# Optimization experiments

Measured on AMD Instinct MI355X. Metric: run time of the kernel, lower is better.

Reference implementation:

```python
import jax, jax.numpy as jnp
import numpy as np

D_IN, D_HID = 64, 128

def _ff(x, w1, b1, w2, b2):
    # FeedForward: Linear -> ReLU -> Linear
    return jax.nn.relu(x @ w1 + b1) @ w2 + b2

def setup_inputs() -> dict:
    key = jax.random.key(0)
    ks = jax.random.split(key, 10)
    N, m = 8, 2048
    def lin(k, fan_in, fan_out):
        bound = 1.0 / np.sqrt(fan_in)
        return jax.random.uniform(k, (fan_in, fan_out), jnp.float32, -bound, bound)
    return {
        "x": jax.random.normal(ks[0], (N, m, D_IN), jnp.float32),
        "edge": jax.random.uniform(ks[1], (N, m, m), jnp.float32),
        # f: dim_in -> dim_hid//2 -> dim_hid
        "f_w1": lin(ks[2], D_IN, D_HID // 2),
        "f_b1": jnp.zeros((D_HID // 2,), jnp.float32),
        "f_w2": lin(ks[3], D_HID // 2, D_HID),
        "f_b2": jnp.zeros((D_HID,), jnp.float32),
        # g: 2*dim_in -> dim_hid -> dim_hid
        "g_w1": lin(ks[4], 2 * D_IN, D_HID),
        "g_b1": jnp.zeros((D_HID,), jnp.float32),
        "g_w2": lin(ks[5], D_HID, D_HID),
        "g_b2": jnp.zeros((D_HID,), jnp.float32),
    }

def reference(x, edge, f_w1, f_b1, f_w2, f_b2, g_w1, g_b1, g_w2, g_b2):
    # self dynamics: f(x) -> [N, m, D_HID]
    self_dyn = _ff(x, f_w1, f_b1, f_w2, f_b2)
    # Original builds interaction[n,i,j] = cat(x[n,i], x[n,i]) (receiver is
    # transposed twice), so g is constant along j. Compute g once per sender node.
    gx = _ff(jnp.concatenate([x, x], axis=-1), g_w1, g_b1, g_w2, g_b2)  # [N, m, H]
    # interaction.sum over sender dim i with edge weights: out[n,j] = sum_i edge[n,i,j]*gx[n,i]
    inter = jnp.einsum('nij,nih->njh', edge, gx)
    return self_dyn + inter
```

## Files before the change

kernel.cpp:

```cpp
#include <hip/hip_runtime.h>


typedef __attribute__((ext_vector_type(8))) short bf16x8;
typedef __attribute__((ext_vector_type(4))) unsigned short u16x4;
typedef __attribute__((ext_vector_type(4))) float f32x4;

static __device__ __forceinline__ unsigned short f2bf(float f) {
  union { float f; unsigned int i; } c; c.f = f;
  return (unsigned short)((c.i + 0x7fffu + ((c.i >> 16) & 1u)) >> 16);
}

__global__ __launch_bounds__(256) void k_gx(
    const float* __restrict__ x,
    const float* __restrict__ gw1,
    const float* __restrict__ gb1,
    const float* __restrict__ gw2,
    const float* __restrict__ gb2,
    unsigned short* __restrict__ gxT)
{
  __shared__ short xs[64 * 64];
  __shared__ short w1T[128 * 64];
  __shared__ short w2T[128 * 128];
  __shared__ short h2s[64 * 128];

  const int t = threadIdx.x;
  const int R0 = blockIdx.x * 64;

  for (int idx = t; idx < 64 * 128; idx += 256) {
    int k = idx >> 7, n = idx & 127;
    float v = gw1[idx] + gw1[64 * 128 + idx];
    w1T[(n << 6) + (((k >> 3) ^ (n & 7)) << 3) + (k & 7)] = (short)f2bf(v);
  }
  for (int idx = t; idx < 128 * 128; idx += 256) {
    int k = idx >> 7, n = idx & 127;
    w2T[(n << 7) + (((k >> 3) ^ (n & 7)) << 3) + (k & 7)] = (short)f2bf(gw2[idx]);
  }
  for (int s = t; s < 64 * 16; s += 256) {
    int row = s >> 4, c4 = s & 15;
    f32x4 v = *(const f32x4*)(x + (size_t)(R0 + row) * 64 + c4 * 4);
    u16x4 pk;
#pragma unroll
    for (int r = 0; r < 4; ++r) pk[r] = f2bf(v[r]);
    *(u16x4*)(xs + (row << 6) + (((c4 >> 1) ^ (row & 7)) << 3) + ((c4 & 1) << 2)) = pk;
  }
  __syncthreads();

  const int w = t >> 6, l = t & 63;
  const int lr = l & 15, q = l >> 4;
  const int mrow = w * 16 + lr;

  bf16x8 a[2];
#pragma unroll
  for (int ks = 0; ks < 2; ++ks) {
    int c = ks * 4 + q;
    a[ks] = *(const bf16x8*)(xs + (mrow << 6) + ((c ^ (mrow & 7)) << 3));
  }

  f32x4 acc;
#pragma unroll
  for (int nf = 0; nf < 8; ++nf) {
    acc = (f32x4){0.f, 0.f, 0.f, 0.f};
#pragma unroll
    for (int ks = 0; ks < 2; ++ks) {
      int c = ks * 4 + q;
      int nr = nf * 16 + lr;
      bf16x8 b = *(const bf16x8*)(w1T + (nr << 6) + ((c ^ (nr & 7)) << 3));
      acc = __builtin_amdgcn_mfma_f32_16x16x32_bf16(a[ks], b, acc, 0, 0, 0);
    }
    float bias = gb1[nf * 16 + lr];
#pragma unroll
    for (int r = 0; r < 4; ++r) {
      float v = acc[r] + bias;
      v = v > 0.f ? v : 0.f;
      int row = w * 16 + q * 4 + r, n = nf * 16 + lr;
      h2s[(row << 7) + (((n >> 3) ^ (row & 7)) << 3) + (n & 7)] = (short)f2bf(v);
    }
  }
  __syncthreads();

  bf16x8 a2[4];
#pragma unroll
  for (int ks = 0; ks < 4; ++ks) {
    int c = ks * 4 + q;
    a2[ks] = *(const bf16x8*)(h2s + (mrow << 7) + ((c ^ (mrow & 7)) << 3));
  }
  const int batch = R0 >> 11;
  const int ib = R0 & 2047;
#pragma unroll
  for (int nf = 0; nf < 8; ++nf) {
    acc = (f32x4){0.f, 0.f, 0.f, 0.f};
#pragma unroll
    for (int ks = 0; ks < 4; ++ks) {
      int c = ks * 4 + q;
      int nr = nf * 16 + lr;
      bf16x8 b = *(const bf16x8*)(w2T + (nr << 7) + ((c ^ (nr & 7)) << 3));
      acc = __builtin_amdgcn_mfma_f32_16x16x32_bf16(a2[ks], b, acc, 0, 0, 0);
    }
    float bias = gb2[nf * 16 + lr];
    u16x4 pk;
#pragma unroll
    for (int r = 0; r < 4; ++r) pk[r] = f2bf(acc[r] + bias);
    *(u16x4*)(gxT + (size_t)(batch * 128 + nf * 16 + lr) * 2048 + ib + w * 16 + q * 4) = pk;
  }
}

__global__ __launch_bounds__(256, 4) void k_main(
    const float* __restrict__ edge,
    const unsigned short* __restrict__ gxT,
    const float* __restrict__ x,
    const float* __restrict__ fw1,
    const float* __restrict__ fb1,
    const float* __restrict__ fw2,
    const float* __restrict__ fb2,
    float* __restrict__ out)
{
  __shared__ short eT[2][16 * 72];
  __shared__ short bT[128 * 64];
  __shared__ short xs[16 * 64];
  __shared__ short w1T[64 * 64];
  __shared__ short h1s[16 * 64];

  const int t = threadIdx.x;
  const int batch = blockIdx.x & 7;
  const int j0 = (blockIdx.x >> 3) * 16;

  const int w = t >> 6, l = t & 63;
  const int lr = l & 15, q = l >> 4;

  const int e_ii = t >> 2;
  const int e_cj = t & 3;

  const float* ep = edge + (size_t)batch * 2048 * 2048 + (size_t)e_ii * 2048 + j0 + e_cj * 4;
  const unsigned short* gp = gxT + ((size_t)batch * 128 + w * 32 + lr) * 2048 + q * 8;

  f32x4 acc[2];
#pragma unroll
  for (int nf = 0; nf < 2; ++nf) acc[nf] = (f32x4){0.f, 0.f, 0.f, 0.f};

  auto lde = [&](int kk, f32x4& er) {
    er = *(const f32x4*)(ep + (size_t)kk * 64 * 2048);
  };
  auto ldg = [&](int kk, bf16x8 gf[4]) {
    const unsigned short* p = gp + kk * 64;
#pragma unroll
    for (int nf = 0; nf < 2; ++nf)
#pragma unroll
      for (int ks = 0; ks < 2; ++ks)
        gf[nf * 2 + ks] = *(const bf16x8*)(p + nf * 16 * 2048 + ks * 32);
  };
  auto st_e = [&](int buf, const f32x4& er) {
#pragma unroll
    for (int u = 0; u < 4; ++u) {
      int jj = e_cj * 4 + u;
      eT[buf][jj * 72 + (((e_ii >> 3) ^ (jj >> 3)) << 3) + (e_ii & 7)] = (short)f2bf(er[u]);
    }
  };
  auto comp = [&](int buf, const bf16x8 gf[4]) {
#pragma unroll
    for (int ks = 0; ks < 2; ++ks) {
      const int c = ks * 4 + q;
      bf16x8 a = *(const bf16x8*)(&eT[buf][lr * 72 + ((c ^ (lr >> 3)) << 3)]);
#pragma unroll
      for (int nf = 0; nf < 2; ++nf)
        acc[nf] = __builtin_amdgcn_mfma_f32_16x16x32_bf16(a, gf[nf * 2 + ks], acc[nf], 0, 0, 0);
    }
  };

  f32x4 erA, erB;
  bf16x8 gfA[4], gfB[4];

  lde(0, erA);
  ldg(0, gfA);
  lde(1, erB);
  st_e(0, erA);
  __syncthreads();

#pragma unroll 1
  for (int mm = 0; mm < 15; ++mm) {
    ldg(2 * mm + 1, gfB);
    lde(2 * mm + 2, erA);
    comp(0, gfA);
    st_e(1, erB);
    __syncthreads();
    ldg(2 * mm + 2, gfA);
    lde(2 * mm + 3, erB);
    comp(1, gfB);
    st_e(0, erA);
    __syncthreads();
  }
  ldg(31, gfB);
  comp(0, gfA);
  st_e(1, erB);
  __syncthreads();
  comp(1, gfB);

  for (int idx = t; idx < 64 * 64; idx += 256) {
    int k = idx >> 6, n = idx & 63;
    w1T[(n << 6) + (((k >> 3) ^ (n & 7)) << 3) + (k & 7)] = (short)f2bf(fw1[idx]);
  }
  for (int idx = t; idx < 64 * 128; idx += 256) {
    int k = idx >> 7, n = idx & 127;
    bT[(n << 6) + (((k >> 3) ^ (n & 7)) << 3) + (k & 7)] = (short)f2bf(fw2[idx]);
  }
  {
    int s = t;
    int row = s >> 4, c4 = s & 15;
    f32x4 v = *(const f32x4*)(x + (size_t)(batch * 2048 + j0 + row) * 64 + c4 * 4);
    u16x4 pk;
#pragma unroll
    for (int r = 0; r < 4; ++r) pk[r] = f2bf(v[r]);
    *(u16x4*)(xs + (row << 6) + (((c4 >> 1) ^ (row & 7)) << 3) + ((c4 & 1) << 2)) = pk;
  }
  __syncthreads();

  if (w == 0) {
    bf16x8 a1[2];
#pragma unroll
    for (int ks = 0; ks < 2; ++ks) {
      int c = ks * 4 + q;
      a1[ks] = *(const bf16x8*)(xs + (lr << 6) + ((c ^ (lr & 7)) << 3));
    }
#pragma unroll
    for (int nf = 0; nf < 4; ++nf) {
      f32x4 h = (f32x4){0.f, 0.f, 0.f, 0.f};
#pragma unroll
      for (int ks = 0; ks < 2; ++ks) {
        int c = ks * 4 + q;
        int nr = nf * 16 + lr;
        bf16x8 b = *(const bf16x8*)(w1T + (nr << 6) + ((c ^ (nr & 7)) << 3));
        h = __builtin_amdgcn_mfma_f32_16x16x32_bf16(a1[ks], b, h, 0, 0, 0);
      }
      float bias = fb1[nf * 16 + lr];
#pragma unroll
      for (int r = 0; r < 4; ++r) {
        float v = h[r] + bias;
        v = v > 0.f ? v : 0.f;
        int row = q * 4 + r, n = nf * 16 + lr;
        h1s[(row << 6) + (((n >> 3) ^ (row & 7)) << 3) + (n & 7)] = (short)f2bf(v);
      }
    }
  }
  __syncthreads();

  bf16x8 a2[2];
#pragma unroll
  for (int ks = 0; ks < 2; ++ks) {
    int c = ks * 4 + q;
    a2[ks] = *(const bf16x8*)(h1s + (lr << 6) + ((c ^ (lr & 7)) << 3));
  }
#pragma unroll
  for (int nf = 0; nf < 2; ++nf) {
    int h = w * 32 + nf * 16 + lr;
#pragma unroll
    for (int ks = 0; ks < 2; ++ks) {
      int c = ks * 4 + q;
      bf16x8 b = *(const bf16x8*)(bT + (h << 6) + ((c ^ (h & 7)) << 3));
      acc[nf] = __builtin_amdgcn_mfma_f32_16x16x32_bf16(a2[ks], b, acc[nf], 0, 0, 0);
    }
    float bias = fb2[h];
#pragma unroll
    for (int r = 0; r < 4; ++r) {
      size_t o = ((size_t)batch * 2048 + j0 + q * 4 + r) * 128 + h;
      out[o] = acc[nf][r] + bias;
    }
  }
}

extern "C" void kernel_launch(void* const* d_in, const int* in_sizes, int n_in,
                              void* d_out, int out_size, void* d_ws, size_t ws_size,
                              hipStream_t stream) {
  const float* x    = (const float*)d_in[0];
  const float* edge = (const float*)d_in[1];
  const float* fw1  = (const float*)d_in[2];
  const float* fb1  = (const float*)d_in[3];
  const float* fw2  = (const float*)d_in[4];
  const float* fb2  = (const float*)d_in[5];
  const float* gw1  = (const float*)d_in[6];
  const float* gb1  = (const float*)d_in[7];
  const float* gw2  = (const float*)d_in[8];
  const float* gb2  = (const float*)d_in[9];
  float* out = (float*)d_out;

  unsigned short* gxT = (unsigned short*)d_ws;

  hipLaunchKernelGGL(k_gx, dim3(256), dim3(256), 0, stream, x, gw1, gb1, gw2, gb2, gxT);
  hipLaunchKernelGGL(k_main, dim3(1024), dim3(256), 0, stream, edge, gxT, x,
                     fw1, fb1, fw2, fb2, out);
}
```

Before: 281.4 us.

## Store gx in MFMA fragment order, vectorize weight loads, lighten barriers, raise MFMA priority

The k_gx kernel now writes gx in a pre-swizzled fragment layout, so each lane in k_main reads its bf16x8 operands with fully contiguous, coalesced loads instead of strided rows. Weight staging in k_gx uses float4 loads. The pipeline barriers in k_main drop __syncthreads for an LDS-only waitcnt plus s_barrier, so outstanding global loads are not drained at each barrier, and MFMA sections run at raised wave priority. The risk is that the lighter barrier depends on the producer and consumer layouts staying exactly consistent.

```diff
diff --git a/kernel.cpp b/kernel.cpp
--- a/kernel.cpp
+++ b/kernel.cpp
@@ -9,6 +9,11 @@
   union { float f; unsigned int i; } c; c.f = f;
   return (unsigned short)((c.i + 0x7fffu + ((c.i >> 16) & 1u)) >> 16);
 }
+
+#define LBAR() do { \
+  asm volatile("s_waitcnt lgkmcnt(0)" ::: "memory"); \
+  __builtin_amdgcn_s_barrier(); \
+} while (0)
 
 __global__ __launch_bounds__(256) void k_gx(
     const float* __restrict__ x,
@@ -16,7 +21,7 @@
     const float* __restrict__ gb1,
     const float* __restrict__ gw2,
     const float* __restrict__ gb2,
-    unsigned short* __restrict__ gxT)
+    unsigned short* __restrict__ gxF)
 {
   __shared__ short xs[64 * 64];
   __shared__ short w1T[128 * 64];
@@ -26,14 +31,24 @@
   const int t = threadIdx.x;
   const int R0 = blockIdx.x * 64;
 
-  for (int idx = t; idx < 64 * 128; idx += 256) {
-    int k = idx >> 7, n = idx & 127;
-    float v = gw1[idx] + gw1[64 * 128 + idx];
-    w1T[(n << 6) + (((k >> 3) ^ (n & 7)) << 3) + (k & 7)] = (short)f2bf(v);
-  }
-  for (int idx = t; idx < 128 * 128; idx += 256) {
-    int k = idx >> 7, n = idx & 127;
-    w2T[(n << 7) + (((k >> 3) ^ (n & 7)) << 3) + (k & 7)] = (short)f2bf(gw2[idx]);
+  for (int idx4 = t; idx4 < 64 * 32; idx4 += 256) {
+    int k = idx4 >> 5, n0 = (idx4 & 31) << 2;
+    f32x4 v1 = *(const f32x4*)(gw1 + (idx4 << 2));
+    f32x4 v2 = *(const f32x4*)(gw1 + 64 * 128 + (idx4 << 2));
+#pragma unroll
+    for (int r = 0; r < 4; ++r) {
+      int n = n0 + r;
+      w1T[(n << 6) + (((k >> 3) ^ (n & 7)) << 3) + (k & 7)] = (short)f2bf(v1[r] + v2[r]);
+    }
+  }
+  for (int idx4 = t; idx4 < 128 * 32; idx4 += 256) {
+    int k = idx4 >> 5, n0 = (idx4 & 31) << 2;
+    f32x4 v = *(const f32x4*)(gw2 + (idx4 << 2));
+#pragma unroll
+    for (int r = 0; r < 4; ++r) {
+      int n = n0 + r;
+      w2T[(n << 7) + (((k >> 3) ^ (n & 7)) << 3) + (k & 7)] = (short)f2bf(v[r]);
+    }
   }
   for (int s = t; s < 64 * 16; s += 256) {
     int row = s >> 4, c4 = s & 15;
@@ -85,7 +100,10 @@
     a2[ks] = *(const bf16x8*)(h2s + (mrow << 7) + ((c ^ (mrow & 7)) << 3));
   }
   const int batch = R0 >> 11;
-  const int ib = R0 & 2047;
+  const int kk = (R0 & 2047) >> 6;
+  unsigned short* gbase = gxF + (size_t)batch * (128 * 2048) + (size_t)kk * (128 * 64);
+  const int cch = w * 2 + (q >> 1);
+  const int ks2 = cch >> 2, qq = cch & 3, r8 = (q & 1) * 4;
 #pragma unroll
   for (int nf = 0; nf < 8; ++nf) {
     acc = (f32x4){0.f, 0.f, 0.f, 0.f};
@@ -100,13 +118,13 @@
     u16x4 pk;
 #pragma unroll
     for (int r = 0; r < 4; ++r) pk[r] = f2bf(acc[r] + bias);
-    *(u16x4*)(gxT + (size_t)(batch * 128 + nf * 16 + lr) * 2048 + ib + w * 16 + q * 4) = pk;
+    *(u16x4*)(gbase + (((nf * 2 + ks2) * 64 + qq * 16 + lr) << 3) + r8) = pk;
   }
 }
 
 __global__ __launch_bounds__(256, 4) void k_main(
     const float* __restrict__ edge,
-    const unsigned short* __restrict__ gxT,
+    const unsigned short* __restrict__ gxF,
     const float* __restrict__ x,
     const float* __restrict__ fw1,
     const float* __restrict__ fb1,
@@ -131,7 +149,7 @@
   const int e_cj = t & 3;
 
   const float* ep = edge + (size_t)batch * 2048 * 2048 + (size_t)e_ii * 2048 + j0 + e_cj * 4;
-  const unsigned short* gp = gxT + ((size_t)batch * 128 + w * 32 + lr) * 2048 + q * 8;
+  const unsigned short* gp = gxF + (size_t)batch * (128 * 2048) + w * 2048 + (size_t)l * 8;
 
   f32x4 acc[2];
 #pragma unroll
@@ -141,12 +159,12 @@
     er = *(const f32x4*)(ep + (size_t)kk * 64 * 2048);
   };
   auto ldg = [&](int kk, bf16x8 gf[4]) {
-    const unsigned short* p = gp + kk * 64;
+    const unsigned short* p = gp + kk * 8192;
 #pragma unroll
     for (int nf = 0; nf < 2; ++nf)
 #pragma unroll
       for (int ks = 0; ks < 2; ++ks)
-        gf[nf * 2 + ks] = *(const bf16x8*)(p + nf * 16 * 2048 + ks * 32);
+        gf[nf * 2 + ks] = *(const bf16x8*)(p + nf * 1024 + ks * 512);
   };
   auto st_e = [&](int buf, const f32x4& er) {
 #pragma unroll
@@ -156,6 +174,7 @@
     }
   };
   auto comp = [&](int buf, const bf16x8 gf[4]) {
+    __builtin_amdgcn_s_setprio(1);
 #pragma unroll
     for (int ks = 0; ks < 2; ++ks) {
       const int c = ks * 4 + q;
@@ -164,6 +183,7 @@
       for (int nf = 0; nf < 2; ++nf)
         acc[nf] = __builtin_amdgcn_mfma_f32_16x16x32_bf16(a, gf[nf * 2 + ks], acc[nf], 0, 0, 0);
     }
+    __builtin_amdgcn_s_setprio(0);
   };
 
   f32x4 erA, erB;
@@ -173,7 +193,7 @@
   ldg(0, gfA);
   lde(1, erB);
   st_e(0, erA);
-  __syncthreads();
+  LBAR();
 
 #pragma unroll 1
   for (int mm = 0; mm < 15; ++mm) {
@@ -181,17 +201,17 @@
     lde(2 * mm + 2, erA);
     comp(0, gfA);
     st_e(1, erB);
-    __syncthreads();
+    LBAR();
     ldg(2 * mm + 2, gfA);
     lde(2 * mm + 3, erB);
     comp(1, gfB);
     st_e(0, erA);
-    __syncthreads();
+    LBAR();
   }
   ldg(31, gfB);
   comp(0, gfA);
   st_e(1, erB);
-  __syncthreads();
+  LBAR();
   comp(1, gfB);
 
   for (int idx = t; idx < 64 * 64; idx += 256) {
@@ -281,9 +301,9 @@
   const float* gb2  = (const float*)d_in[9];
   float* out = (float*)d_out;
 
-  unsigned short* gxT = (unsigned short*)d_ws;
-
-  hipLaunchKernelGGL(k_gx, dim3(256), dim3(256), 0, stream, x, gw1, gb1, gw2, gb2, gxT);
-  hipLaunchKernelGGL(k_main, dim3(1024), dim3(256), 0, stream, edge, gxT, x,
+  unsigned short* gxF = (unsigned short*)d_ws;
+
+  hipLaunchKernelGGL(k_gx, dim3(256), dim3(256), 0, stream, x, gw1, gb1, gw2, gb2, gxF);
+  hipLaunchKernelGGL(k_main, dim3(1024), dim3(256), 0, stream, edge, gxF, x,
                      fw1, fb1, fw2, fb2, out);
 }
```

New measurement: 265.6 us. 5.6% less time.
